# Kernel tuning notes

Measured on AMD Instinct MI355X. Metric: run time of the kernel, lower is better.

The kernel has to match this reference:

```python
import jax, jax.numpy as jnp
import numpy as np

# Model constants (match init_kwargs)
V_SIZE = 6144
D = 1024
K = 32            # SNN frames per token
N_LAYERS = 4
B = 2
S = 256
SUR_ALPHA = 4.0   # surrogate sigmoid alpha (dynamic _mpd_alpha affects grads only; fixed here)


def rmsnorm(x, w, eps=1e-6):
    return x * jax.lax.rsqrt(jnp.mean(x * x, axis=-1, keepdims=True) + eps) * w


def plif_scan(beta, u, v_th, alpha_sur):
    """PLIF row-param parallel scan: V[t] = beta*V[t-1] + u[t] (v_init = 0),
    spike[t] = Heaviside(V[t] - v_th) with sigmoid surrogate (straight-through).
    u: (T, B, D); beta, v_th: broadcastable to (B, D)."""
    A = jnp.broadcast_to(beta, u.shape)

    def comb(c1, c2):
        a1, b1 = c1
        a2, b2 = c2
        return a1 * a2, a2 * b1 + b2

    _, V = jax.lax.associative_scan(comb, (A, u))  # linear first-order recurrence
    vs = V - v_th
    sg = jax.nn.sigmoid(alpha_sur * vs)
    spike = jax.lax.stop_gradient((vs >= 0).astype(u.dtype) - sg) + sg
    return spike


def setup_inputs() -> dict:
    key = jax.random.key(0)
    ks = jax.random.split(key, 8)
    sc = 1.0 / np.sqrt(D)
    inp = {}
    inp["token_ids"] = jax.random.randint(ks[0], (B, S), 0, V_SIZE)
    inp["embed"] = jax.random.normal(ks[1], (V_SIZE, D), jnp.float32) * 0.02
    inp["W_in"] = jax.random.normal(ks[2], (N_LAYERS, D, D), jnp.float32) * sc
    inp["W_out"] = jax.random.normal(ks[3], (N_LAYERS, D, D), jnp.float32) * sc
    inp["layer_beta"] = jnp.full((N_LAYERS, D), 0.5, jnp.float32)  # tau=2 -> decay 0.5
    inp["layer_vth"] = jnp.full((N_LAYERS, D), 0.3, jnp.float32)
    inp["out_norm_w"] = jnp.ones((D,), jnp.float32)
    inp["out_beta"] = jnp.full((D,), 0.5, jnp.float32)
    inp["out_vth"] = jnp.full((D,), 0.3, jnp.float32)
    inp["out_alpha"] = jnp.ones((1,), jnp.float32)
    inp["decode_w"] = jax.random.normal(ks[4], (D, D), jnp.float32) * sc
    inp["decode_b"] = jnp.zeros((D,), jnp.float32)
    inp["li_norm_w"] = jnp.ones((D,), jnp.float32)
    return inp


def reference(token_ids, embed, W_in, W_out, layer_beta, layer_vth,
              out_norm_w, out_beta, out_vth, out_alpha,
              decode_w, decode_b, li_norm_w):
    b, s = token_ids.shape
    # encode: embed lookup, repeat each token K times -> (T=s*K, b, D)
    emb = embed[token_ids]                                   # (b, s, D)
    x = jnp.repeat(emb[:, :, None, :], K, axis=2)            # (b, s, K, D)
    x = x.reshape(b, s * K, D).transpose(1, 0, 2)            # (T, b, D)
    # SNN decoder layers (PLIF recurrence + residual projections)
    for i in range(N_LAYERS):
        u = jnp.einsum('tbd,de->tbe', x, W_in[i])
        spike = plif_scan(layer_beta[i], u, layer_vth[i], SUR_ALPHA)
        x = x + jnp.einsum('tbd,de->tbe', spike * layer_vth[i], W_out[i])
    # decode: RMSNorm -> output PLIF neuron parallel scan -> spike current
    h = rmsnorm(x, out_norm_w)
    spike = plif_scan(out_beta, out_alpha * h, out_vth, SUR_ALPHA)
    v_out = spike * out_vth                                  # spike_current_activation
    # K-frame aggregation: (T, b, D) -> (s, K, b, D) -> mean over K -> (b, s, D)
    decoded = v_out.reshape(s, K, b, D).mean(axis=1).transpose(1, 0, 2)
    h2 = decoded @ decode_w.T + decode_b                     # decode_proj
    h2 = rmsnorm(h2, li_norm_w)                              # LateralInhibition norm
    return h2 @ embed.T                                      # tied LM head -> (b, s, V)
```

## Files before the change

kernel.cpp:

```cpp
#include <hip/hip_runtime.h>

typedef __bf16 bf16x8 __attribute__((ext_vector_type(8)));
typedef __bf16 bf16x4 __attribute__((ext_vector_type(4)));
typedef __bf16 bf16x2 __attribute__((ext_vector_type(2)));
typedef float  f32x4  __attribute__((ext_vector_type(4)));
typedef float  f32x16 __attribute__((ext_vector_type(16)));

constexpr int Bc = 2, Sc = 256, Kc = 32, Tc = 8192, Dc = 1024, Vc = 6144, NLc = 4;
constexpr int NPANEL = (Tc * Bc) / 128;
constexpr int UTS = NLc * Dc;

__device__ __forceinline__ void gload16(const void* g, void* l) {
    __builtin_amdgcn_global_load_lds(
        (const __attribute__((address_space(1))) unsigned int*)g,
        (__attribute__((address_space(3))) unsigned int*)l,
        16, 0, 0);
}

__device__ __forceinline__ int xcd_swz(int lin, int nwg) {
    int q = nwg >> 3, r = nwg & 7;
    int x = lin & 7, o = lin >> 3;
    int base = (x < r) ? x * (q + 1) : r * (q + 1) + (x - r) * q;
    return base + o;
}

__device__ __forceinline__ bool gate_or(const int* f, int n, int p) {
    bool g = false;
    for (int j = 0; j < n; ++j) g = g || (f[j * NPANEL + p] != 0);
    return g;
}

template<int EPI, int BM, int BN, int BK>
__global__ __launch_bounds__(256)
void gemm_bt(const __bf16* __restrict__ A, const __bf16* __restrict__ BT,
             int M, int N, int Kd,
             float* __restrict__ Cout, __bf16* __restrict__ outb,
             const float* __restrict__ bias)
{
    constexpr int MI = BM / 32, NI = BN / 32;
    constexpr int KCH  = BK / 8;
    constexpr int SWM  = KCH - 1;
    constexpr int ROWB = BK * 2;
    constexpr int CA = BM * KCH / 256;
    constexpr int CB = BN * KCH / 256;
    __shared__ char lds[(BM + BN) * ROWB];
    char* As = lds;
    char* Bs = lds + BM * ROWB;
    const int tid  = threadIdx.x;
    const int lane = tid & 63;
    const int wid  = tid >> 6;
    const int wm   = wid & 1, wn = wid >> 1;

    const int nwg = gridDim.x * gridDim.y;
    const int lin = blockIdx.y * gridDim.x + blockIdx.x;
    const int swz = xcd_swz(lin, nwg);
    const int bn  = (swz % gridDim.x) * BN;
    const int bm  = (swz / gridDim.x) * BM;

    const __bf16* asrc[CA];
#pragma unroll
    for (int i = 0; i < CA; ++i) {
        int chunk = i * 256 + tid;
        int row = chunk / KCH, kc = chunk % KCH;
        int kcs = kc ^ (row & SWM);
        asrc[i] = A + (size_t)(bm + row) * Kd + kcs * 8;
    }
    const __bf16* bsrc[CB];
#pragma unroll
    for (int i = 0; i < CB; ++i) {
        int chunk = i * 256 + tid;
        int row = chunk / KCH, kc = chunk % KCH;
        int kcs = kc ^ (row & SWM);
        bsrc[i] = BT + (size_t)(bn + row) * Kd + kcs * 8;
    }

    f32x4 acc[MI][NI] = {};

    for (int kt = 0; kt < Kd; kt += BK) {
#pragma unroll
        for (int i = 0; i < CA; ++i)
            gload16(asrc[i] + kt, As + (i * 256 + tid) * 16);
#pragma unroll
        for (int i = 0; i < CB; ++i)
            gload16(bsrc[i] + kt, Bs + (i * 256 + tid) * 16);
        __syncthreads();
#pragma unroll
        for (int kk = 0; kk < BK / 32; ++kk) {
            const int ko = kk * 64 + ((lane >> 4) << 4);
            bf16x8 af[MI], bfr[NI];
#pragma unroll
            for (int mi = 0; mi < MI; ++mi) {
                int row = wm * (BM / 2) + mi * 16 + (lane & 15);
                af[mi] = *(const bf16x8*)(As + row * ROWB +
                                          (ko ^ ((row & SWM) << 4)));
            }
#pragma unroll
            for (int ni = 0; ni < NI; ++ni) {
                int row = wn * (BN / 2) + ni * 16 + (lane & 15);
                bfr[ni] = *(const bf16x8*)(Bs + row * ROWB +
                                           (ko ^ ((row & SWM) << 4)));
            }
#pragma unroll
            for (int mi = 0; mi < MI; ++mi)
#pragma unroll
                for (int ni = 0; ni < NI; ++ni)
                    acc[mi][ni] = __builtin_amdgcn_mfma_f32_16x16x32_bf16(
                        af[mi], bfr[ni], acc[mi][ni], 0, 0, 0);
        }
        __syncthreads();
    }

    const int cc = lane & 15, cr = (lane >> 4) * 4;
#pragma unroll
    for (int mi = 0; mi < MI; ++mi) {
#pragma unroll
        for (int ni = 0; ni < NI; ++ni) {
            int gcol = bn + wn * (BN / 2) + ni * 16 + cc;
#pragma unroll
            for (int r = 0; r < 4; ++r) {
                int grow = bm + wm * (BM / 2) + mi * 16 + cr + r;
                size_t idx = (size_t)grow * N + gcol;
                float v = acc[mi][ni][r];
                if (EPI == 0)      Cout[idx] = v;
                else if (EPI == 2) Cout[idx] = v + bias[gcol];
                else               outb[idx] = (__bf16)v;
            }
        }
    }
}

template<int EPI, int BK>
__global__ __launch_bounds__(256)
void gemm32(const __bf16* __restrict__ A, const __bf16* __restrict__ BT,
            int M, int N, int Kd,
            float* __restrict__ Cout, __bf16* __restrict__ outb)
{
    constexpr int BM = 64, BN = 64;
    constexpr int KCH  = BK / 8;
    constexpr int SWM  = KCH - 1;
    constexpr int ROWB = BK * 2;
    constexpr int CA = BM * KCH / 256;
    constexpr int CB = BN * KCH / 256;
    __shared__ char lds[(BM + BN) * ROWB];
    char* As = lds;
    char* Bs = lds + BM * ROWB;
    const int tid  = threadIdx.x;
    const int lane = tid & 63;
    const int wid  = tid >> 6;
    const int wm   = wid & 1, wn = wid >> 1;

    const int nwg = gridDim.x * gridDim.y;
    const int lin = blockIdx.y * gridDim.x + blockIdx.x;
    const int swz = xcd_swz(lin, nwg);
    const int bn  = (swz % gridDim.x) * BN;
    const int bm  = (swz / gridDim.x) * BM;

    const __bf16* asrc[CA];
#pragma unroll
    for (int i = 0; i < CA; ++i) {
        int chunk = i * 256 + tid;
        int row = chunk / KCH, kc = chunk % KCH;
        int kcs = kc ^ (row & SWM);
        asrc[i] = A + (size_t)(bm + row) * Kd + kcs * 8;
    }
    const __bf16* bsrc[CB];
#pragma unroll
    for (int i = 0; i < CB; ++i) {
        int chunk = i * 256 + tid;
        int row = chunk / KCH, kc = chunk % KCH;
        int kcs = kc ^ (row & SWM);
        bsrc[i] = BT + (size_t)(bn + row) * Kd + kcs * 8;
    }

    f32x16 acc = {};
    const int arow = wm * 32 + (lane & 31);
    const int brow = wn * 32 + (lane & 31);
    const int kg   = (lane >> 5) << 4;

    for (int kt = 0; kt < Kd; kt += BK) {
#pragma unroll
        for (int i = 0; i < CA; ++i)
            gload16(asrc[i] + kt, As + (i * 256 + tid) * 16);
#pragma unroll
        for (int i = 0; i < CB; ++i)
            gload16(bsrc[i] + kt, Bs + (i * 256 + tid) * 16);
        __syncthreads();
#pragma unroll
        for (int kk = 0; kk < BK / 16; ++kk) {
            const int ko = kk * 32 + kg;
            bf16x8 af = *(const bf16x8*)(As + arow * ROWB +
                                         (ko ^ ((arow & SWM) << 4)));
            bf16x8 bfr = *(const bf16x8*)(Bs + brow * ROWB +
                                          (ko ^ ((brow & SWM) << 4)));
            acc = __builtin_amdgcn_mfma_f32_32x32x16_bf16(af, bfr, acc, 0, 0, 0);
        }
        __syncthreads();
    }

    const int gcol = bn + wn * 32 + (lane & 31);
    const int rbase = bm + wm * 32 + 4 * (lane >> 5);
#pragma unroll
    for (int r = 0; r < 16; ++r) {
        int grow = rbase + (r & 3) + 8 * (r >> 2);
        size_t idx = (size_t)grow * N + gcol;
        if (EPI == 0) Cout[idx] = acc[r];
        else          outb[idx] = (__bf16)acc[r];
    }
}

__global__ __launch_bounds__(256)
void gemm_u_cast(const __bf16* __restrict__ A, const __bf16* __restrict__ BT,
                 __bf16* __restrict__ outb,
                 const float* __restrict__ embed, __bf16* __restrict__ emb_bf)
{
    constexpr int BM = 64, BN = 64, BK = 256;
    constexpr int GX = UTS / BN;
    constexpr int NGEMM = GX * (Bc * Sc / BM);
    constexpr int KCH  = BK / 8, SWM = KCH - 1, ROWB = BK * 2;
    constexpr int CA = BM * KCH / 256, CB = BN * KCH / 256;
    const int tid = threadIdx.x;

    if (blockIdx.x >= NGEMM) {
        int idx = (blockIdx.x - NGEMM) * 256 + tid;
        const f32x4* pp = (const f32x4*)embed + (size_t)idx * 2;
        f32x4 v0 = pp[0], v1 = pp[1];
        bf16x8 o;
        o[0]=(__bf16)v0[0]; o[1]=(__bf16)v0[1]; o[2]=(__bf16)v0[2]; o[3]=(__bf16)v0[3];
        o[4]=(__bf16)v1[0]; o[5]=(__bf16)v1[1]; o[6]=(__bf16)v1[2]; o[7]=(__bf16)v1[3];
        ((bf16x8*)emb_bf)[idx] = o;
        return;
    }

    __shared__ char lds[(BM + BN) * ROWB];
    char* As = lds;
    char* Bs = lds + BM * ROWB;
    const int lane = tid & 63;
    const int wid  = tid >> 6;
    const int wm   = wid & 1, wn = wid >> 1;
    const int swz = xcd_swz(blockIdx.x, NGEMM);
    const int bn  = (swz % GX) * BN;
    const int bm  = (swz / GX) * BM;
    const int Kd  = Dc, N = UTS;

    const __bf16* asrc[CA];
#pragma unroll
    for (int i = 0; i < CA; ++i) {
        int chunk = i * 256 + tid;
        int row = chunk / KCH, kc = chunk % KCH;
        int kcs = kc ^ (row & SWM);
        asrc[i] = A + (size_t)(bm + row) * Kd + kcs * 8;
    }
    const __bf16* bsrc[CB];
#pragma unroll
    for (int i = 0; i < CB; ++i) {
        int chunk = i * 256 + tid;
        int row = chunk / KCH, kc = chunk % KCH;
        int kcs = kc ^ (row & SWM);
        bsrc[i] = BT + (size_t)(bn + row) * Kd + kcs * 8;
    }

    f32x16 acc = {};
    const int arow = wm * 32 + (lane & 31);
    const int brow = wn * 32 + (lane & 31);
    const int kg   = (lane >> 5) << 4;

    for (int kt = 0; kt < Kd; kt += BK) {
#pragma unroll
        for (int i = 0; i < CA; ++i)
            gload16(asrc[i] + kt, As + (i * 256 + tid) * 16);
#pragma unroll
        for (int i = 0; i < CB; ++i)
            gload16(bsrc[i] + kt, Bs + (i * 256 + tid) * 16);
        __syncthreads();
#pragma unroll
        for (int kk = 0; kk < BK / 16; ++kk) {
            const int ko = kk * 32 + kg;
            bf16x8 af = *(const bf16x8*)(As + arow * ROWB +
                                         (ko ^ ((arow & SWM) << 4)));
            bf16x8 bfr = *(const bf16x8*)(Bs + brow * ROWB +
                                          (ko ^ ((brow & SWM) << 4)));
            acc = __builtin_amdgcn_mfma_f32_32x32x16_bf16(af, bfr, acc, 0, 0, 0);
        }
        __syncthreads();
    }

    const int gcol = bn + wn * 32 + (lane & 31);
    const int rbase = bm + wm * 32 + 4 * (lane >> 5);
#pragma unroll
    for (int r = 0; r < 16; ++r) {
        int grow = rbase + (r & 3) + 8 * (r >> 2);
        outb[(size_t)grow * N + gcol] = (__bf16)acc[r];
    }
}

__global__ __launch_bounds__(1024)
void spec_scan(const __bf16* __restrict__ utok_base,
               const float* __restrict__ lbeta, const float* __restrict__ lvth,
               const float* __restrict__ htok, const float* __restrict__ alpha_p,
               const float* __restrict__ obeta, const float* __restrict__ ovth,
               __bf16* __restrict__ decoded, int* __restrict__ flags,
               int* __restrict__ dirtyAny)
{
    const int e = threadIdx.x;
    const int p = blockIdx.x;
    __shared__ int fm;
    if (e == 0) fm = 0;
    __syncthreads();

    unsigned mybits = 0;
#pragma unroll
    for (int l = 0; l < NLc; ++l) {
        const __bf16* utok = utok_base + (size_t)l * Dc;
        const float bet = lbeta[l * Dc + e], vt = lvth[l * Dc + e];
        float a = bet, S = 1.0f;
#pragma unroll
        for (int i = 0; i < 5; ++i) { S = S * (1.0f + a); a = a * a; }
        bool spike = false;
        for (int b = 0; b < Bc; ++b) {
            float V = 0.f;
            if (p > 0) {
#pragma unroll
                for (int ti = 0; ti < 2; ++ti) {
                    float u = (float)utok[((size_t)(2 * p - 2 + ti) * Bc + b) * UTS + e];
                    V = fmaf(a, V, u * S);
                }
            }
#pragma unroll
            for (int ti = 0; ti < 2; ++ti) {
                float u = (float)utok[((size_t)(2 * p + ti) * Bc + b) * UTS + e];
                float V1 = fmaf(bet, V, u);
                V = fmaf(a, V, u * S);
                spike = spike || (fmaxf(V1, V) >= vt);
            }
        }
        if (spike) mybits |= 1u << l;
    }
    unsigned wor = 0;
#pragma unroll
    for (int l = 0; l < NLc; ++l)
        if (__any(mybits & (1u << l))) wor |= 1u << l;
    if ((e & 63) == 0 && wor) atomicOr(&fm, (int)wor);
    __syncthreads();
    const int f = fm;
    if (e < NLc) flags[e * NPANEL + p] = (f >> e) & 1;
    if (e == 0 && f) atomicOr(dirtyAny, 1);

    const int w = e >> 6, lane = e & 63;
    const int ridx = w & 3, cq = w >> 2;
    const int s = 2 * p + (ridx >> 1), b = ridx & 1;
    const int gi = lane + 64 * cq;
    const float al = alpha_p[0];
    const f32x4 obet = ((const f32x4*)obeta)[gi];
    const f32x4 ovt  = ((const f32x4*)ovth)[gi];
    f32x4 oa = obet, oS = {1.f, 1.f, 1.f, 1.f};
#pragma unroll
    for (int i = 0; i < 5; ++i) {
#pragma unroll
        for (int c = 0; c < 4; ++c) { oS[c] *= 1.0f + oa[c]; oa[c] *= oa[c]; }
    }
    f32x4 V = {0, 0, 0, 0}, sum = {0, 0, 0, 0};
    for (int tk = (s >= 2 ? s - 2 : 0); tk < s; ++tk) {
        f32x4 h = ((const f32x4*)(htok + ((size_t)tk * Bc + b) * Dc))[gi];
#pragma unroll
        for (int c = 0; c < 4; ++c) V[c] = fmaf(oa[c], V[c], al * h[c] * oS[c]);
    }
    f32x4 h = ((const f32x4*)(htok + ((size_t)s * Bc + b) * Dc))[gi];
    for (int k = 0; k < Kc; ++k) {
#pragma unroll
        for (int c = 0; c < 4; ++c) {
            V[c] = fmaf(obet[c], V[c], al * h[c]);
            sum[c] += (V[c] >= ovt[c]) ? ovt[c] : 0.f;
        }
    }
    bf16x4 o;
#pragma unroll
    for (int c = 0; c < 4; ++c) o[c] = (__bf16)(sum[c] * (1.0f / 32.0f));
    ((bf16x4*)(decoded + ((size_t)b * Sc + s) * Dc))[gi] = o;
}

__global__ __launch_bounds__(1024)
void fallback_layers(const __bf16* __restrict__ utok_base,
                     const float* __restrict__ W_in, const float* __restrict__ W_out,
                     const float* __restrict__ lbeta, const float* __restrict__ lvth,
                     __bf16* __restrict__ dxA, __bf16* __restrict__ dxB,
                     int* __restrict__ flags_all, const int* __restrict__ dirty)
{
    if (dirty[0] == 0) return;
    const int e = threadIdx.x;
    __shared__ int fm;
    __shared__ __bf16 srow[Dc];
    const __bf16* dxR = dxA;
    __bf16*       dxW = dxB;

    for (int l = 0; l < NLc; ++l) {
        const __bf16* utok = utok_base + (size_t)l * Dc;
        const float*  Win  = W_in  + (size_t)l * Dc * Dc;
        const float*  Wout = W_out + (size_t)l * Dc * Dc;
        const float bet = lbeta[l * Dc + e], vt = lvth[l * Dc + e];
        float a = bet, S = 1.0f;
#pragma unroll
        for (int i = 0; i < 5; ++i) { S = S * (1.0f + a); a = a * a; }
        int* flags_l = flags_all + l * NPANEL;
        const __bf16 vtb = (__bf16)vt, zb = (__bf16)0.f;

        for (int p = 0; p < NPANEL; ++p) {
            const int t0 = p * 64;
            __syncthreads();
            if (e == 0) fm = 0;
            __syncthreads();
            const bool pd  = gate_or(flags_all, l, p);
            const bool pdw = (p > 0) && gate_or(flags_all, l, p - 1);

            auto ut = [&](int tk, int b) -> float {
                return (float)utok[((size_t)tk * Bc + b) * UTS + e];
            };
            auto du_at = [&](int t, int b) -> float {
                __syncthreads();
                srow[e] = dxR[((size_t)t * Bc + b) * Dc + e];
                __syncthreads();
                float acc = 0.f;
                for (int d = 0; d < Dc; ++d)
                    acc = fmaf((float)srow[d], Win[(size_t)d * Dc + e], acc);
                return acc;
            };

            bool spike = false;
            for (int b = 0; b < Bc; ++b) {
                float V = 0.f;
                if (p > 0) {
                    if (!pdw) {
                        for (int ti = 0; ti < 2; ++ti)
                            V = fmaf(a, V, ut(2 * p - 2 + ti, b) * S);
                    } else {
                        for (int t = t0 - 64; t < t0; ++t)
                            V = fmaf(bet, V, ut(t >> 5, b) + du_at(t, b));
                    }
                }
                if (!pd) {
                    for (int ti = 0; ti < 2; ++ti) {
                        const float u = ut(2 * p + ti, b);
                        float V1 = fmaf(bet, V, u);
                        V = fmaf(a, V, u * S);
                        spike = spike || (fmaxf(V1, V) >= vt);
                    }
                } else {
                    for (int k = 0; k < 64; ++k) {
                        V = fmaf(bet, V, ut((t0 + k) >> 5, b) + du_at(t0 + k, b));
                        spike = spike || (V >= vt);
                    }
                }
            }
            if (__any(spike) && (e & 63) == 0) atomicOr(&fm, 1);
            __syncthreads();
            const bool f = (fm != 0);
            if (e == 0) flags_l[p] = f ? 1 : 0;
            __syncthreads();

            if (!f) {
                if (pd) {
                    for (int rr = 0; rr < 128; ++rr)
                        dxW[(size_t)(t0 * Bc + rr) * Dc + e] =
                            dxR[(size_t)(t0 * Bc + rr) * Dc + e];
                }
                continue;
            }
            for (int b = 0; b < Bc; ++b) {
                float V = 0.f;
                if (p > 0) {
                    if (!pdw) {
                        for (int ti = 0; ti < 2; ++ti)
                            V = fmaf(a, V, ut(2 * p - 2 + ti, b) * S);
                    } else {
                        for (int t = t0 - 64; t < t0; ++t)
                            V = fmaf(bet, V, ut(t >> 5, b) + du_at(t, b));
                    }
                }
                for (int k = 0; k < 64; ++k) {
                    const int t = t0 + k;
                    float u = ut(t >> 5, b);
                    if (pd) u += du_at(t, b);
                    V = fmaf(bet, V, u);
                    __syncthreads();
                    srow[e] = (V >= vt) ? vtb : zb;
                    __syncthreads();
                    float acc2 = 0.f;
                    for (int d = 0; d < Dc; ++d)
                        acc2 = fmaf((float)srow[d], Wout[(size_t)d * Dc + e], acc2);
                    size_t r = (size_t)t * Bc + b;
                    float base = pd ? (float)dxR[r * Dc + e] : 0.f;
                    dxW[r * Dc + e] = (__bf16)(base + acc2);
                }
            }
        }
        __bf16* tmpw = dxW;
        dxW = (__bf16*)dxR;
        dxR = tmpw;
        __syncthreads();
    }
}

__global__ __launch_bounds__(256)
void out_scan2(const float* __restrict__ htok, const __bf16* __restrict__ dxf,
               const int* __restrict__ tok, const float* __restrict__ embed,
               const float* __restrict__ onw, const float* __restrict__ alpha_p,
               const float* __restrict__ obeta, const float* __restrict__ ovth,
               const int* __restrict__ flags, __bf16* __restrict__ decoded,
               const int* __restrict__ dirtyp)
{
    if (dirtyp[0] == 0) return;
    const int tid = threadIdx.x;
    const int s = blockIdx.x, b = blockIdx.y;
    const float al = alpha_p[0];
    const f32x4 bet = ((const f32x4*)obeta)[tid];
    const f32x4 vt  = ((const f32x4*)ovth)[tid];
    f32x4 a = bet, S = {1.f, 1.f, 1.f, 1.f};
#pragma unroll
    for (int i = 0; i < 5; ++i) {
#pragma unroll
        for (int c = 0; c < 4; ++c) { S[c] *= 1.0f + a[c]; a[c] *= a[c]; }
    }

    const int t0 = s * Kc;
    const int tlo = (t0 >= 64) ? t0 - 64 : 0;
    bool dirty = false;
    for (int c = tlo >> 6; c <= (t0 + Kc - 1) >> 6; ++c)
        dirty = dirty || gate_or(flags, NLc, c);

    f32x4 V = {0,0,0,0}, sum = {0,0,0,0};
    if (!dirty) {
        for (int tk = (s >= 2 ? s - 2 : 0); tk < s; ++tk) {
            f32x4 h = ((const f32x4*)(htok + ((size_t)tk * Bc + b) * Dc))[tid];
#pragma unroll
            for (int c = 0; c < 4; ++c) V[c] = fmaf(a[c], V[c], al * h[c] * S[c]);
        }
        f32x4 h = ((const f32x4*)(htok + ((size_t)s * Bc + b) * Dc))[tid];
        for (int k = 0; k < Kc; ++k) {
#pragma unroll
            for (int c = 0; c < 4; ++c) {
                V[c] = fmaf(bet[c], V[c], al * h[c]);
                sum[c] += (V[c] >= vt[c]) ? vt[c] : 0.f;
            }
        }
    } else {
        const f32x4 wv = ((const f32x4*)onw)[tid];
        __shared__ float red[4];
        for (int t = tlo; t < t0 + Kc; ++t) {
            const bool g = gate_or(flags, NLc, t >> 6);
            f32x4 h;
            if (g) {
                size_t r = (size_t)t * Bc + b;
                int id = tok[b * Sc + (t >> 5)];
                f32x4 v = ((const f32x4*)(embed + (size_t)id * Dc))[tid];
                bf16x4 dv = ((const bf16x4*)(dxf + r * Dc))[tid];
#pragma unroll
                for (int c = 0; c < 4; ++c) v[c] += (float)dv[c];
                float ss = v[0]*v[0] + v[1]*v[1] + v[2]*v[2] + v[3]*v[3];
#pragma unroll
                for (int off = 32; off >= 1; off >>= 1) ss += __shfl_down(ss, off);
                if ((tid & 63) == 0) red[tid >> 6] = ss;
                __syncthreads();
                float tot = red[0] + red[1] + red[2] + red[3];
                __syncthreads();
                float sc = rsqrtf(tot * (1.0f / Dc) + 1e-6f);
#pragma unroll
                for (int c = 0; c < 4; ++c) h[c] = v[c] * sc * wv[c];
            } else {
                h = ((const f32x4*)(htok + ((size_t)(t >> 5) * Bc + b) * Dc))[tid];
            }
#pragma unroll
            for (int c = 0; c < 4; ++c) {
                V[c] = fmaf(bet[c], V[c], al * h[c]);
                if (t >= t0) sum[c] += (V[c] >= vt[c]) ? vt[c] : 0.f;
            }
        }
    }
    bf16x4 o;
#pragma unroll
    for (int c = 0; c < 4; ++c) o[c] = (__bf16)(sum[c] * (1.0f / 32.0f));
    ((bf16x4*)(decoded + ((size_t)b * Sc + s) * Dc))[tid] = o;
}

__global__ __launch_bounds__(256)
void prep(const float* __restrict__ W_in, const float* __restrict__ embed,
          const float* __restrict__ decode_w, const int* __restrict__ tok,
          const float* __restrict__ onw, __bf16* __restrict__ wT_in,
          __bf16* __restrict__ decw_bf,
          __bf16* __restrict__ xtok, float* __restrict__ h_tok,
          int* __restrict__ flags)
{
    const int blk = blockIdx.x;
    const int tid = threadIdx.x;
    if (blk < 4096) {
        __shared__ float tile[32][33];
        const int mat = blk >> 10;
        const int t2  = blk & 1023;
        const int d0  = (t2 & 31) * 32, e0 = (t2 >> 5) * 32;
        const float* Wm = W_in + (size_t)mat * Dc * Dc;
        __bf16*      Wo = wT_in + (size_t)mat * Dc * Dc;
        const int tx = tid & 31, ty = tid >> 5;
#pragma unroll
        for (int i = 0; i < 4; ++i)
            tile[ty + i*8][tx] = Wm[(size_t)(d0 + ty + i*8) * Dc + e0 + tx];
        __syncthreads();
        const int txp = tid & 15, tyw = tid >> 4;
#pragma unroll
        for (int i = 0; i < 2; ++i) {
            int r = tyw + 16 * i;
            bf16x2 o;
            o[0] = (__bf16)tile[2*txp][r];
            o[1] = (__bf16)tile[2*txp + 1][r];
            *(bf16x2*)(&Wo[(size_t)(e0 + r) * Dc + d0 + 2*txp]) = o;
        }
    } else if (blk < 4608) {
        int idx = (blk - 4096) * 256 + tid;
        const f32x4* pp = (const f32x4*)decode_w + (size_t)idx * 2;
        f32x4 v0 = pp[0], v1 = pp[1];
        bf16x8 o;
        o[0]=(__bf16)v0[0]; o[1]=(__bf16)v0[1]; o[2]=(__bf16)v0[2]; o[3]=(__bf16)v0[3];
        o[4]=(__bf16)v1[0]; o[5]=(__bf16)v1[1]; o[6]=(__bf16)v1[2]; o[7]=(__bf16)v1[3];
        ((bf16x8*)decw_bf)[idx] = o;
    } else {
        const int r = blk - 4608;
        if (r == 0) {
            flags[tid] = 0; flags[tid + 256] = 0;
            if (tid == 0) flags[512] = 0;
        }
        const int s = r >> 1, b = r & 1;
        const int id = tok[b * Sc + s];
        const f32x4 v = ((const f32x4*)(embed + (size_t)id * Dc))[tid];
        float ss = v[0]*v[0] + v[1]*v[1] + v[2]*v[2] + v[3]*v[3];
#pragma unroll
        for (int off = 32; off >= 1; off >>= 1) ss += __shfl_down(ss, off);
        __shared__ float red[4];
        if ((tid & 63) == 0) red[tid >> 6] = ss;
        __syncthreads();
        float tot = red[0] + red[1] + red[2] + red[3];
        float sc = rsqrtf(tot * (1.0f / Dc) + 1e-6f);
        const f32x4 wv = ((const f32x4*)onw)[tid];
        bf16x4 o; o[0]=(__bf16)v[0]; o[1]=(__bf16)v[1]; o[2]=(__bf16)v[2]; o[3]=(__bf16)v[3];
        ((bf16x4*)(xtok + (size_t)r * Dc))[tid] = o;
        f32x4 h = {v[0]*sc*wv[0], v[1]*sc*wv[1], v[2]*sc*wv[2], v[3]*sc*wv[3]};
        ((f32x4*)(h_tok + (size_t)r * Dc))[tid] = h;
    }
}

__global__ __launch_bounds__(256)
void rmsnorm_rows(const float* __restrict__ in, const float* __restrict__ w,
                  __bf16* __restrict__ outb)
{
    const int r = blockIdx.x;
    const int tid = threadIdx.x;
    const f32x4 v = ((const f32x4*)(in + (size_t)r * Dc))[tid];
    float ss = v[0]*v[0] + v[1]*v[1] + v[2]*v[2] + v[3]*v[3];
#pragma unroll
    for (int off = 32; off >= 1; off >>= 1) ss += __shfl_down(ss, off);
    __shared__ float red[4];
    if ((tid & 63) == 0) red[tid >> 6] = ss;
    __syncthreads();
    float tot = red[0] + red[1] + red[2] + red[3];
    float sc = rsqrtf(tot * (1.0f / Dc) + 1e-6f);
    const f32x4 wv = ((const f32x4*)w)[tid];
    bf16x4 o;
    o[0]=(__bf16)(v[0]*sc*wv[0]); o[1]=(__bf16)(v[1]*sc*wv[1]);
    o[2]=(__bf16)(v[2]*sc*wv[2]); o[3]=(__bf16)(v[3]*sc*wv[3]);
    ((bf16x4*)(outb + (size_t)r * Dc))[tid] = o;
}

extern "C" void kernel_launch(void* const* d_in, const int* in_sizes, int n_in,
                              void* d_out, int out_size, void* d_ws, size_t ws_size,
                              hipStream_t stream)
{
    const int*   token_ids  = (const int*)  d_in[0];
    const float* embed      = (const float*)d_in[1];
    const float* W_in       = (const float*)d_in[2];
    const float* W_out      = (const float*)d_in[3];
    const float* layer_beta = (const float*)d_in[4];
    const float* layer_vth  = (const float*)d_in[5];
    const float* out_norm_w = (const float*)d_in[6];
    const float* out_beta   = (const float*)d_in[7];
    const float* out_vth    = (const float*)d_in[8];
    const float* out_alpha  = (const float*)d_in[9];
    const float* decode_w   = (const float*)d_in[10];
    const float* decode_b   = (const float*)d_in[11];
    const float* li_norm_w  = (const float*)d_in[12];
    float* out = (float*)d_out;

    size_t off = 0;
    auto alloc = [&](size_t bytes) -> void* {
        void* p = (char*)d_ws + off;
        off += (bytes + 255) & ~(size_t)255;
        return p;
    };
    __bf16* dxA      = (__bf16*)alloc((size_t)Tc * Bc * Dc * 2);
    __bf16* dxB      = (__bf16*)alloc((size_t)Tc * Bc * Dc * 2);
    __bf16* u_tokall = (__bf16*)alloc((size_t)Bc * Sc * UTS * 2);
    float*  h_tok    = (float*) alloc((size_t)Bc * Sc * Dc * 4);
    __bf16* xtok     = (__bf16*)alloc((size_t)Bc * Sc * Dc * 2);
    __bf16* wT_in    = (__bf16*)alloc((size_t)NLc * Dc * Dc * 2);
    __bf16* emb_bf   = (__bf16*)alloc((size_t)Vc * Dc * 2);
    __bf16* decw_bf  = (__bf16*)alloc((size_t)Dc * Dc * 2);
    __bf16* decoded  = (__bf16*)alloc((size_t)Bc * Sc * Dc * 2);
    float*  h2       = (float*) alloc((size_t)Bc * Sc * Dc * 4);
    __bf16* h2n      = (__bf16*)alloc((size_t)Bc * Sc * Dc * 2);
    int*    flags    = (int*)   alloc(((size_t)NLc * NPANEL + 64) * 4);
    int*    dirtyAny = flags + NLc * NPANEL;

    prep<<<5120, 256, 0, stream>>>(W_in, embed, decode_w, token_ids, out_norm_w,
                                   wT_in, decw_bf, xtok, h_tok, flags);

    gemm_u_cast<<<512 + Vc * Dc / 8 / 256, 256, 0, stream>>>(
        xtok, wT_in, u_tokall, embed, emb_bf);

    spec_scan<<<NPANEL, 1024, 0, stream>>>(
        u_tokall, layer_beta, layer_vth, h_tok, out_alpha, out_beta, out_vth,
        decoded, flags, dirtyAny);

    fallback_layers<<<1, 1024, 0, stream>>>(
        u_tokall, W_in, W_out, layer_beta, layer_vth, dxA, dxB, flags, dirtyAny);
    out_scan2<<<dim3(Sc, Bc), 256, 0, stream>>>(
        h_tok, dxA, token_ids, embed, out_norm_w, out_alpha, out_beta, out_vth,
        flags, decoded, dirtyAny);

    gemm_bt<2, 32, 64, 256><<<dim3(Dc / 64, (Bc * Sc) / 32), 256, 0, stream>>>(
        decoded, decw_bf, Bc * Sc, Dc, Dc, h2, nullptr, decode_b);
    rmsnorm_rows<<<Bc * Sc, 256, 0, stream>>>(h2, li_norm_w, h2n);
    gemm32<0, 128><<<dim3(Vc / 64, (Bc * Sc) / 64), 256, 0, stream>>>(
        h2n, emb_bf, Bc * Sc, Vc, Dc, out, nullptr);
}
```

Baseline: 70.22 us.

## Fuse decode bias and RMSNorm into GEMM epilogues, drop rmsnorm kernel

The decode-projection GEMM epilogue now adds the bias, writes the h2 values already scaled by the norm weight as bf16, and accumulates per-row sums of squares into a buffer using wave shuffles and atomics. The LM-head GEMM then applies the per-row rsqrt scale in its epilogue. This removes the separate rmsnorm kernel launch and the fp32 h2 round trip through memory. In exchange it adds atomics, non-deterministic summation order, and one bf16 rounding applied before normalisation rather than after.

Result: slower. 74.81 us (+6.5%).

```diff
diff --git a/kernel.cpp b/kernel.cpp
--- a/kernel.cpp
+++ b/kernel.cpp
@@ -30,12 +30,12 @@
     return g;
 }
 
-template<int EPI, int BM, int BN, int BK>
+template<int BM, int BN, int BK>
 __global__ __launch_bounds__(256)
-void gemm_bt(const __bf16* __restrict__ A, const __bf16* __restrict__ BT,
-             int M, int N, int Kd,
-             float* __restrict__ Cout, __bf16* __restrict__ outb,
-             const float* __restrict__ bias)
+void gemm_dec(const __bf16* __restrict__ A, const __bf16* __restrict__ BT,
+              int M, int N, int Kd,
+              __bf16* __restrict__ h2w, const float* __restrict__ bias,
+              const float* __restrict__ liw, float* __restrict__ rowss)
 {
     constexpr int MI = BM / 32, NI = BN / 32;
     constexpr int KCH  = BK / 8;
@@ -116,24 +116,28 @@
 #pragma unroll
         for (int ni = 0; ni < NI; ++ni) {
             int gcol = bn + wn * (BN / 2) + ni * 16 + cc;
+            float bz = bias[gcol], lw = liw[gcol];
 #pragma unroll
             for (int r = 0; r < 4; ++r) {
                 int grow = bm + wm * (BM / 2) + mi * 16 + cr + r;
-                size_t idx = (size_t)grow * N + gcol;
-                float v = acc[mi][ni][r];
-                if (EPI == 0)      Cout[idx] = v;
-                else if (EPI == 2) Cout[idx] = v + bias[gcol];
-                else               outb[idx] = (__bf16)v;
-            }
-        }
-    }
-}
-
-template<int EPI, int BK>
+                float v = acc[mi][ni][r] + bz;
+                h2w[(size_t)grow * N + gcol] = (__bf16)(v * lw);
+                float ss = v * v;
+#pragma unroll
+                for (int off = 8; off >= 1; off >>= 1)
+                    ss += __shfl_down(ss, off);
+                if (cc == 0 && ((lane >> 4) == (lane >> 4)))
+                    atomicAdd(&rowss[grow], ss);
+            }
+        }
+    }
+}
+
+template<int BK>
 __global__ __launch_bounds__(256)
-void gemm32(const __bf16* __restrict__ A, const __bf16* __restrict__ BT,
-            int M, int N, int Kd,
-            float* __restrict__ Cout, __bf16* __restrict__ outb)
+void gemm_head(const __bf16* __restrict__ A, const __bf16* __restrict__ BT,
+               int M, int N, int Kd,
+               float* __restrict__ Cout, const float* __restrict__ rowss)
 {
     constexpr int BM = 64, BN = 64;
     constexpr int KCH  = BK / 8;
@@ -202,9 +206,8 @@
 #pragma unroll
     for (int r = 0; r < 16; ++r) {
         int grow = rbase + (r & 3) + 8 * (r >> 2);
-        size_t idx = (size_t)grow * N + gcol;
-        if (EPI == 0) Cout[idx] = acc[r];
-        else          outb[idx] = (__bf16)acc[r];
+        float sc = rsqrtf(rowss[grow] * (1.0f / Dc) + 1e-6f);
+        Cout[(size_t)grow * N + gcol] = acc[r] * sc;
     }
 }
 
@@ -586,7 +589,7 @@
           const float* __restrict__ onw, __bf16* __restrict__ wT_in,
           __bf16* __restrict__ decw_bf,
           __bf16* __restrict__ xtok, float* __restrict__ h_tok,
-          int* __restrict__ flags)
+          int* __restrict__ flags, float* __restrict__ rowss)
 {
     const int blk = blockIdx.x;
     const int tid = threadIdx.x;
@@ -624,6 +627,8 @@
         if (r == 0) {
             flags[tid] = 0; flags[tid + 256] = 0;
             if (tid == 0) flags[512] = 0;
+        } else if (r == 1) {
+            rowss[tid] = 0.f; rowss[tid + 256] = 0.f;
         }
         const int s = r >> 1, b = r & 1;
         const int id = tok[b * Sc + s];
@@ -642,28 +647,6 @@
         f32x4 h = {v[0]*sc*wv[0], v[1]*sc*wv[1], v[2]*sc*wv[2], v[3]*sc*wv[3]};
         ((f32x4*)(h_tok + (size_t)r * Dc))[tid] = h;
     }
-}
-
-__global__ __launch_bounds__(256)
-void rmsnorm_rows(const float* __restrict__ in, const float* __restrict__ w,
-                  __bf16* __restrict__ outb)
-{
-    const int r = blockIdx.x;
-    const int tid = threadIdx.x;
-    const f32x4 v = ((const f32x4*)(in + (size_t)r * Dc))[tid];
-    float ss = v[0]*v[0] + v[1]*v[1] + v[2]*v[2] + v[3]*v[3];
-#pragma unroll
-    for (int off = 32; off >= 1; off >>= 1) ss += __shfl_down(ss, off);
-    __shared__ float red[4];
-    if ((tid & 63) == 0) red[tid >> 6] = ss;
-    __syncthreads();
-    float tot = red[0] + red[1] + red[2] + red[3];
-    float sc = rsqrtf(tot * (1.0f / Dc) + 1e-6f);
-    const f32x4 wv = ((const f32x4*)w)[tid];
-    bf16x4 o;
-    o[0]=(__bf16)(v[0]*sc*wv[0]); o[1]=(__bf16)(v[1]*sc*wv[1]);
-    o[2]=(__bf16)(v[2]*sc*wv[2]); o[3]=(__bf16)(v[3]*sc*wv[3]);
-    ((bf16x4*)(outb + (size_t)r * Dc))[tid] = o;
 }
 
 extern "C" void kernel_launch(void* const* d_in, const int* in_sizes, int n_in,
@@ -700,13 +683,13 @@
     __bf16* emb_bf   = (__bf16*)alloc((size_t)Vc * Dc * 2);
     __bf16* decw_bf  = (__bf16*)alloc((size_t)Dc * Dc * 2);
     __bf16* decoded  = (__bf16*)alloc((size_t)Bc * Sc * Dc * 2);
-    float*  h2       = (float*) alloc((size_t)Bc * Sc * Dc * 4);
-    __bf16* h2n      = (__bf16*)alloc((size_t)Bc * Sc * Dc * 2);
+    __bf16* h2w      = (__bf16*)alloc((size_t)Bc * Sc * Dc * 2);
+    float*  rowss    = (float*) alloc((size_t)Bc * Sc * 4);
     int*    flags    = (int*)   alloc(((size_t)NLc * NPANEL + 64) * 4);
     int*    dirtyAny = flags + NLc * NPANEL;
 
     prep<<<5120, 256, 0, stream>>>(W_in, embed, decode_w, token_ids, out_norm_w,
-                                   wT_in, decw_bf, xtok, h_tok, flags);
+                                   wT_in, decw_bf, xtok, h_tok, flags, rowss);
 
     gemm_u_cast<<<512 + Vc * Dc / 8 / 256, 256, 0, stream>>>(
         xtok, wT_in, u_tokall, embed, emb_bf);
@@ -721,9 +704,8 @@
         h_tok, dxA, token_ids, embed, out_norm_w, out_alpha, out_beta, out_vth,
         flags, decoded, dirtyAny);
 
-    gemm_bt<2, 32, 64, 256><<<dim3(Dc / 64, (Bc * Sc) / 32), 256, 0, stream>>>(
-        decoded, decw_bf, Bc * Sc, Dc, Dc, h2, nullptr, decode_b);
-    rmsnorm_rows<<<Bc * Sc, 256, 0, stream>>>(h2, li_norm_w, h2n);
-    gemm32<0, 128><<<dim3(Vc / 64, (Bc * Sc) / 64), 256, 0, stream>>>(
-        h2n, emb_bf, Bc * Sc, Vc, Dc, out, nullptr);
-}
+    gemm_dec<32, 64, 256><<<dim3(Dc / 64, (Bc * Sc) / 32), 256, 0, stream>>>(
+        decoded, decw_bf, Bc * Sc, Dc, Dc, h2w, decode_b, li_norm_w, rowss);
+    gemm_head<128><<<dim3(Vc / 64, (Bc * Sc) / 64), 256, 0, stream>>>(
+        h2w, emb_bf, Bc * Sc, Vc, Dc, out, rowss);
+}
```
